# Performance work log

Measured on AMD Instinct MI355X. Metric: run time of the kernel, lower is better.

## Reference

```python
import jax, jax.numpy as jnp
import numpy as np

B, S, D = 4, 2048, 1024
H = 16
DH = D // H  # attention_head_size = 64


def setup_inputs() -> dict:
    key = jax.random.key(0)
    ks = jax.random.split(key, 7)
    scale = 0.02
    return {
        "hidden_states": jax.random.normal(ks[0], (B, S, D), dtype=jnp.float32),
        "Wq": jax.random.normal(ks[1], (D, D), dtype=jnp.float32) * scale,
        "bq": jnp.zeros((D,), dtype=jnp.float32),
        "Wk": jax.random.normal(ks[2], (D, D), dtype=jnp.float32) * scale,
        "bk": jnp.zeros((D,), dtype=jnp.float32),
        "Wv": jax.random.normal(ks[3], (D, D), dtype=jnp.float32) * scale,
        "bv": jnp.zeros((D,), dtype=jnp.float32),
    }


def _split_heads(x):
    # [B, S, D] -> [B, H, S, DH]
    b, s, _ = x.shape
    return x.reshape(b, s, H, DH).transpose(0, 2, 1, 3)


def reference(hidden_states, Wq, bq, Wk, bk, Wv, bv):
    # torch nn.Linear computes x @ W.T + b
    q = _split_heads(hidden_states @ Wq.T + bq)  # [B,H,S,DH]
    k = _split_heads(hidden_states @ Wk.T + bk)
    v = _split_heads(hidden_states @ Wv.T + bv)

    scores = jnp.einsum("bhqd,bhkd->bhqk", q, k) / jnp.sqrt(jnp.float32(DH))
    # original detaches attention probs (LRP-style)
    probs = jax.lax.stop_gradient(jax.nn.softmax(scores, axis=-1))
    ctx = jnp.einsum("bhqk,bhkd->bhqd", probs, v)  # [B,H,S,DH]
    # [B,H,S,DH] -> [B,S,D]
    return ctx.transpose(0, 2, 1, 3).reshape(hidden_states.shape[0], hidden_states.shape[1], D)
```

## Files before the change

### kernel.cpp

```cpp
#include <hip/hip_runtime.h>

typedef _Float16 f16;
typedef f16 f16x2 __attribute__((ext_vector_type(2)));
typedef f16 f16x4 __attribute__((ext_vector_type(4)));
typedef f16 f16x8 __attribute__((ext_vector_type(8)));
typedef float f32x4 __attribute__((ext_vector_type(4)));

#define NB 4
#define NS 2048
#define ND 1024
#define NH 16
#define NDH 64

__device__ __forceinline__ void gl2lds16(const void* g, void* l) {
  __builtin_amdgcn_global_load_lds(
      (const __attribute__((address_space(1))) unsigned int*)g,
      (__attribute__((address_space(3))) unsigned int*)l, 16, 0, 0);
}

__device__ __forceinline__ float fast_exp2(float x) {
  return __builtin_amdgcn_exp2f(x);
}

__device__ __forceinline__ f16x2 pk_f16(float a, float b) {
  return __builtin_bit_cast(f16x2, __builtin_amdgcn_cvt_pkrtz(a, b));
}

__global__ __launch_bounds__(256) void cvt_all(
    const float* __restrict__ X, const float* __restrict__ Wq,
    const float* __restrict__ Wk, const float* __restrict__ Wv,
    f16* __restrict__ Xh, f16* __restrict__ Wh) {
  int b = blockIdx.x;
  const float* src;
  f16* dst;
  int off;
  if (b < 8192)       { src = X;  dst = Xh;               off = 0; }
  else if (b < 9216)  { src = Wq; dst = Wh;               off = 8192; }
  else if (b < 10240) { src = Wk; dst = Wh + (1u << 20);  off = 9216; }
  else                { src = Wv; dst = Wh + (2u << 20);  off = 10240; }
  int i = (b - off) * 256 + threadIdx.x;
  float4 v = ((const float4*)src)[i];
  f16x4 h = {(f16)v.x, (f16)v.y, (f16)v.z, (f16)v.w};
  ((f16x4*)dst)[i] = h;
}

__global__ __launch_bounds__(256) void qkv_gemm(
    const f16* __restrict__ Xh, const f16* __restrict__ Wh,
    const float* __restrict__ bq, const float* __restrict__ bk,
    const float* __restrict__ bv,
    f16* __restrict__ QF, f16* __restrict__ KF, f16* __restrict__ VF) {
  __shared__ f16 Ah[128 * 64];
  __shared__ f16 Bh[128 * 64];
  const int t = threadIdx.x;
  const int tileM = blockIdx.x * 128;
  const int nGlob = blockIdx.y * 128;
  const int mat = nGlob >> 10;
  const int col0 = nGlob & 1023;
  const int wave = t >> 6, lane = t & 63;
  const int mOff = (wave & 1) * 64, nOff = (wave >> 1) * 64;
  const int lr = lane & 15, quad = lane >> 4;

  f32x4 acc[4][4];
#pragma unroll
  for (int i = 0; i < 4; i++)
#pragma unroll
    for (int j = 0; j < 4; j++) acc[i][j] = f32x4{0.f, 0.f, 0.f, 0.f};

  const int srow = t >> 3;
  const int sx = ((t & 7) ^ (srow & 7)) * 8;
  const f16* ag = Xh + (size_t)(tileM + srow) * ND + sx;
  const f16* bg = Wh + (size_t)mat * ND * ND + (size_t)(col0 + srow) * ND + sx;
  const bool qk = (mat < 2);
  const int rx = lr & 7;

  for (int kk = 0; kk < ND; kk += 64) {
    __syncthreads();
    gl2lds16(ag + kk,                       Ah + t * 8);
    gl2lds16(ag + (size_t)32 * ND + kk,     Ah + 2048 + t * 8);
    gl2lds16(ag + (size_t)64 * ND + kk,     Ah + 4096 + t * 8);
    gl2lds16(ag + (size_t)96 * ND + kk,     Ah + 6144 + t * 8);
    gl2lds16(bg + kk,                       Bh + t * 8);
    gl2lds16(bg + (size_t)32 * ND + kk,     Bh + 2048 + t * 8);
    gl2lds16(bg + (size_t)64 * ND + kk,     Bh + 4096 + t * 8);
    gl2lds16(bg + (size_t)96 * ND + kk,     Bh + 6144 + t * 8);
    __syncthreads();
#pragma unroll
    for (int c = 0; c < 2; c++) {
      const int ch = ((c * 4 + quad) ^ rx) * 8;
      f16x8 af[4], bf[4];
#pragma unroll
      for (int i = 0; i < 4; i++)
        af[i] = *(const f16x8*)(Ah + (mOff + i * 16 + lr) * 64 + ch);
#pragma unroll
      for (int j = 0; j < 4; j++)
        bf[j] = *(const f16x8*)(Bh + (nOff + j * 16 + lr) * 64 + ch);
      if (qk) {
#pragma unroll
        for (int i = 0; i < 4; i++)
#pragma unroll
          for (int j = 0; j < 4; j++)
            acc[i][j] = __builtin_amdgcn_mfma_f32_16x16x32_f16(bf[j], af[i], acc[i][j], 0, 0, 0);
      } else {
#pragma unroll
        for (int i = 0; i < 4; i++)
#pragma unroll
          for (int j = 0; j < 4; j++)
            acc[i][j] = __builtin_amdgcn_mfma_f32_16x16x32_f16(af[i], bf[j], acc[i][j], 0, 0, 0);
      }
    }
  }

  if (qk) {
    const float* bias = (mat == 0) ? bq : bk;
    f16* dst = (mat == 0) ? QF : KF;
    const float sc = (mat == 0) ? 0.18033688f : 1.0f;
    const int jstart = (quad & 1) * 4;
#pragma unroll
    for (int j = 0; j < 4; j++) {
      int n0 = col0 + nOff + j * 16;
      int h = n0 >> 6;
      int f = j >> 1;
      int lam = lr + 16 * ((2 * j + (quad >> 1)) & 3);
      float4 bb = *(const float4*)(bias + n0 + quad * 4);
#pragma unroll
      for (int i = 0; i < 4; i++) {
        int sF = tileM + mOff + i * 16;
        int b = sF >> 11, st = (sF & 2047) >> 4;
        int bh = b * NH + h;
        f16x4 v;
#pragma unroll
        for (int r = 0; r < 4; r++) v[r] = (f16)((acc[i][j][r] + (&bb.x)[r]) * sc);
        *(f16x4*)(dst + (((size_t)(bh * 128 + st) * 2 + f) * 64 + lam) * 8 + jstart) = v;
      }
    }
  } else {
#pragma unroll
    for (int j = 0; j < 4; j++) {
      int n = col0 + nOff + j * 16 + lr;
      int h = n >> 6, dt = (n >> 4) & 3;
      float bb = bv[n];
#pragma unroll
      for (int i = 0; i < 4; i++) {
        int sF = tileM + mOff + i * 16;
        int b = sF >> 11;
        int kt2 = (sF & 2047) >> 5;
        int ts = (sF >> 4) & 1;
        int bh = b * NH + h;
        f16x4 v;
#pragma unroll
        for (int r = 0; r < 4; r++) v[r] = (f16)(acc[i][j][r] + bb);
        *(f16x4*)(VF + ((size_t)(bh * 64 + kt2) * 4 + dt) * 512 +
                  (size_t)(quad * 16 + lr) * 8 + 4 * ts) = v;
      }
    }
  }
}

__global__ __launch_bounds__(256, 2) void attn_kernel(
    const f16* __restrict__ QF, const f16* __restrict__ KF,
    const f16* __restrict__ VF, float* __restrict__ out) {
  __shared__ f16 LK[3][2048];
  __shared__ f16 LV[3][2048];
  const int t = threadIdx.x, wave = t >> 6, lane = t & 63;
  const int lr = lane & 15, quad = lane >> 4;
  const int bh = blockIdx.x, qb = blockIdx.y;
  const int bb = bh >> 4, hh = bh & 15;
  const size_t bhOff = (size_t)bh * 131072;
  const f16* Qp = QF + bhOff + (size_t)lane * 8;
  const f16* Kg = KF + bhOff + (size_t)t * 8;
  const f16* Vg = VF + bhOff + (size_t)t * 8;
  const int st0 = qb * 16 + wave * 4;

  f16x8 qf[4][2];
#pragma unroll
  for (int qt = 0; qt < 4; qt++) {
    qf[qt][0] = *(const f16x8*)(Qp + (size_t)(st0 + qt) * 1024);
    qf[qt][1] = *(const f16x8*)(Qp + (size_t)(st0 + qt) * 1024 + 512);
  }

  f32x4 o[4][4];
#pragma unroll
  for (int qt = 0; qt < 4; qt++)
#pragma unroll
    for (int dt = 0; dt < 4; dt++) o[qt][dt] = f32x4{0.f, 0.f, 0.f, 0.f};
  f32x4 lacc[4];
#pragma unroll
  for (int qt = 0; qt < 4; qt++) lacc[qt] = f32x4{0.f, 0.f, 0.f, 0.f};
  const f16x8 ones8 = {(f16)1.f, (f16)1.f, (f16)1.f, (f16)1.f,
                       (f16)1.f, (f16)1.f, (f16)1.f, (f16)1.f};

  f16x8 pfP[4], vvP[4];

  gl2lds16(Kg,        &LK[0][t * 8]);
  gl2lds16(Vg,        &LV[0][t * 8]);
  gl2lds16(Kg + 2048, &LK[1][t * 8]);
  gl2lds16(Vg + 2048, &LV[1][t * 8]);
  asm volatile("s_waitcnt vmcnt(2)" ::: "memory");
  __builtin_amdgcn_s_barrier();

  {
    f16x8 kk[4];
#pragma unroll
    for (int i = 0; i < 4; i++)
      kk[i] = *(const f16x8*)(&LK[0][i * 512 + lane * 8]);
#pragma unroll
    for (int i = 0; i < 4; i++)
      vvP[i] = *(const f16x8*)(&LV[0][i * 512 + lane * 8]);
    gl2lds16(Kg + 2 * 2048, &LK[2][t * 8]);
    gl2lds16(Vg + 2 * 2048, &LV[2][t * 8]);
    f32x4 sA[4], sB[4];
#pragma unroll
    for (int qt = 0; qt < 4; qt++) {
      sA[qt] = f32x4{0.f, 0.f, 0.f, 0.f};
      sA[qt] = __builtin_amdgcn_mfma_f32_16x16x32_f16(kk[0], qf[qt][0], sA[qt], 0, 0, 0);
      sA[qt] = __builtin_amdgcn_mfma_f32_16x16x32_f16(kk[1], qf[qt][1], sA[qt], 0, 0, 0);
      sB[qt] = f32x4{0.f, 0.f, 0.f, 0.f};
      sB[qt] = __builtin_amdgcn_mfma_f32_16x16x32_f16(kk[2], qf[qt][0], sB[qt], 0, 0, 0);
      sB[qt] = __builtin_amdgcn_mfma_f32_16x16x32_f16(kk[3], qf[qt][1], sB[qt], 0, 0, 0);
    }
#pragma unroll
    for (int qt = 0; qt < 4; qt++) {
      f16x2 a0 = pk_f16(fast_exp2(sA[qt][0]), fast_exp2(sA[qt][1]));
      f16x2 a1 = pk_f16(fast_exp2(sA[qt][2]), fast_exp2(sA[qt][3]));
      f16x2 b0 = pk_f16(fast_exp2(sB[qt][0]), fast_exp2(sB[qt][1]));
      f16x2 b1 = pk_f16(fast_exp2(sB[qt][2]), fast_exp2(sB[qt][3]));
      f16x4 lo = __builtin_shufflevector(a0, a1, 0, 1, 2, 3);
      f16x4 hi = __builtin_shufflevector(b0, b1, 0, 1, 2, 3);
      pfP[qt] = __builtin_shufflevector(lo, hi, 0, 1, 2, 3, 4, 5, 6, 7);
    }
  }
  asm volatile("s_waitcnt vmcnt(2)" ::: "memory");
  __builtin_amdgcn_s_barrier();

  int cur = 1;
  for (int g = 1; g < 64; ++g) {
    f16x8 kk[4], vv[4];
#pragma unroll
    for (int i = 0; i < 4; i++)
      kk[i] = *(const f16x8*)(&LK[cur][i * 512 + lane * 8]);
#pragma unroll
    for (int i = 0; i < 4; i++)
      vv[i] = *(const f16x8*)(&LV[cur][i * 512 + lane * 8]);
    {
      int s2 = cur + 2; if (s2 >= 3) s2 -= 3;
      const size_t nk = (size_t)((g + 2) & 63) * 2048;
      gl2lds16(Kg + nk, &LK[s2][t * 8]);
      gl2lds16(Vg + nk, &LV[s2][t * 8]);
    }
    __builtin_amdgcn_s_setprio(1);
#pragma unroll
    for (int dt = 0; dt < 4; dt++)
#pragma unroll
      for (int qt = 0; qt < 4; qt++)
        o[qt][dt] = __builtin_amdgcn_mfma_f32_16x16x32_f16(pfP[qt], vvP[dt], o[qt][dt], 0, 0, 0);
#pragma unroll
    for (int qt = 0; qt < 4; qt++)
      lacc[qt] = __builtin_amdgcn_mfma_f32_16x16x32_f16(pfP[qt], ones8, lacc[qt], 0, 0, 0);
    f32x4 sA[4], sB[4];
#pragma unroll
    for (int qt = 0; qt < 4; qt++) {
      sA[qt] = f32x4{0.f, 0.f, 0.f, 0.f};
      sA[qt] = __builtin_amdgcn_mfma_f32_16x16x32_f16(kk[0], qf[qt][0], sA[qt], 0, 0, 0);
      sA[qt] = __builtin_amdgcn_mfma_f32_16x16x32_f16(kk[1], qf[qt][1], sA[qt], 0, 0, 0);
      sB[qt] = f32x4{0.f, 0.f, 0.f, 0.f};
      sB[qt] = __builtin_amdgcn_mfma_f32_16x16x32_f16(kk[2], qf[qt][0], sB[qt], 0, 0, 0);
      sB[qt] = __builtin_amdgcn_mfma_f32_16x16x32_f16(kk[3], qf[qt][1], sB[qt], 0, 0, 0);
    }
    __builtin_amdgcn_s_setprio(0);
#pragma unroll
    for (int qt = 0; qt < 4; qt++) {
      f16x2 a0 = pk_f16(fast_exp2(sA[qt][0]), fast_exp2(sA[qt][1]));
      f16x2 a1 = pk_f16(fast_exp2(sA[qt][2]), fast_exp2(sA[qt][3]));
      f16x2 b0 = pk_f16(fast_exp2(sB[qt][0]), fast_exp2(sB[qt][1]));
      f16x2 b1 = pk_f16(fast_exp2(sB[qt][2]), fast_exp2(sB[qt][3]));
      f16x4 lo = __builtin_shufflevector(a0, a1, 0, 1, 2, 3);
      f16x4 hi = __builtin_shufflevector(b0, b1, 0, 1, 2, 3);
      pfP[qt] = __builtin_shufflevector(lo, hi, 0, 1, 2, 3, 4, 5, 6, 7);
    }
#pragma unroll
    for (int i = 0; i < 4; i++) vvP[i] = vv[i];
    asm volatile("s_waitcnt vmcnt(2)" ::: "memory");
    __builtin_amdgcn_s_barrier();
    cur = (cur == 2) ? 0 : cur + 1;
  }

#pragma unroll
  for (int dt = 0; dt < 4; dt++)
#pragma unroll
    for (int qt = 0; qt < 4; qt++)
      o[qt][dt] = __builtin_amdgcn_mfma_f32_16x16x32_f16(pfP[qt], vvP[dt], o[qt][dt], 0, 0, 0);
#pragma unroll
  for (int qt = 0; qt < 4; qt++)
    lacc[qt] = __builtin_amdgcn_mfma_f32_16x16x32_f16(pfP[qt], ones8, lacc[qt], 0, 0, 0);

#pragma unroll
  for (int qt = 0; qt < 4; qt++) {
#pragma unroll
    for (int r = 0; r < 4; r++) {
      float inv = 1.0f / lacc[qt][r];
      int q = qb * 256 + wave * 64 + qt * 16 + quad * 4 + r;
#pragma unroll
      for (int dt = 0; dt < 4; dt++)
        out[((size_t)bb * NS + q) * ND + hh * 64 + dt * 16 + lr] = o[qt][dt][r] * inv;
    }
  }
}

extern "C" void kernel_launch(void* const* d_in, const int* in_sizes, int n_in,
                              void* d_out, int out_size, void* d_ws, size_t ws_size,
                              hipStream_t stream) {
  const float* X  = (const float*)d_in[0];
  const float* Wq = (const float*)d_in[1];
  const float* bq = (const float*)d_in[2];
  const float* Wk = (const float*)d_in[3];
  const float* bk = (const float*)d_in[4];
  const float* Wv = (const float*)d_in[5];
  const float* bv = (const float*)d_in[6];
  float* out = (float*)d_out;

  f16* Xh = (f16*)d_ws;
  f16* Wh = (f16*)((char*)d_ws + (size_t)(16u << 20));
  f16* QF = (f16*)((char*)d_ws + (size_t)(22u << 20));
  f16* KF = (f16*)((char*)d_ws + (size_t)(38u << 20));
  f16* VF = (f16*)((char*)d_ws + (size_t)(54u << 20));

  cvt_all<<<11264, 256, 0, stream>>>(X, Wq, Wk, Wv, Xh, Wh);
  qkv_gemm<<<dim3(64, 24), 256, 0, stream>>>(Xh, Wh, bq, bk, bv, QF, KF, VF);
  attn_kernel<<<dim3(64, 8), 256, 0, stream>>>(QF, KF, VF, out);
}
```

Measured before the change: 214.0 us.

## Triple-buffer QKV GEMM LDS tiles with async prefetch two stages ahead

Reworks the QKV projection GEMM main loop from a synchronous single-buffer K=64 step to a three-stage ring of K=32 LDS buffers. Global-to-LDS loads for step g+2 are issued before computing step g, and partial vmcnt waits plus a single barrier per iteration replace the double syncthreads. The aim is to overlap memory latency with MFMA work. It also adds a launch-bounds occupancy hint of 3 blocks per CU. The cost is more barriers per unit of K, a changed LDS swizzle, and wrap-around prefetches that load redundant data in the final iterations.

```diff
diff --git a/kernel.cpp b/kernel.cpp
--- a/kernel.cpp
+++ b/kernel.cpp
@@ -44,13 +44,13 @@
   ((f16x4*)dst)[i] = h;
 }
 
-__global__ __launch_bounds__(256) void qkv_gemm(
+__global__ __launch_bounds__(256, 3) void qkv_gemm(
     const f16* __restrict__ Xh, const f16* __restrict__ Wh,
     const float* __restrict__ bq, const float* __restrict__ bk,
     const float* __restrict__ bv,
     f16* __restrict__ QF, f16* __restrict__ KF, f16* __restrict__ VF) {
-  __shared__ f16 Ah[128 * 64];
-  __shared__ f16 Bh[128 * 64];
+  __shared__ f16 Ah[3][128 * 32];
+  __shared__ f16 Bh[3][128 * 32];
   const int t = threadIdx.x;
   const int tileM = blockIdx.x * 128;
   const int nGlob = blockIdx.y * 128;
@@ -66,48 +66,57 @@
 #pragma unroll
     for (int j = 0; j < 4; j++) acc[i][j] = f32x4{0.f, 0.f, 0.f, 0.f};
 
-  const int srow = t >> 3;
-  const int sx = ((t & 7) ^ (srow & 7)) * 8;
+  const int srow = t >> 2;
+  const int sx = ((t & 3) ^ ((srow >> 1) & 3)) * 8;
   const f16* ag = Xh + (size_t)(tileM + srow) * ND + sx;
   const f16* bg = Wh + (size_t)mat * ND * ND + (size_t)(col0 + srow) * ND + sx;
   const bool qk = (mat < 2);
-  const int rx = lr & 7;
-
-  for (int kk = 0; kk < ND; kk += 64) {
-    __syncthreads();
-    gl2lds16(ag + kk,                       Ah + t * 8);
-    gl2lds16(ag + (size_t)32 * ND + kk,     Ah + 2048 + t * 8);
-    gl2lds16(ag + (size_t)64 * ND + kk,     Ah + 4096 + t * 8);
-    gl2lds16(ag + (size_t)96 * ND + kk,     Ah + 6144 + t * 8);
-    gl2lds16(bg + kk,                       Bh + t * 8);
-    gl2lds16(bg + (size_t)32 * ND + kk,     Bh + 2048 + t * 8);
-    gl2lds16(bg + (size_t)64 * ND + kk,     Bh + 4096 + t * 8);
-    gl2lds16(bg + (size_t)96 * ND + kk,     Bh + 6144 + t * 8);
-    __syncthreads();
-#pragma unroll
-    for (int c = 0; c < 2; c++) {
-      const int ch = ((c * 4 + quad) ^ rx) * 8;
-      f16x8 af[4], bf[4];
+  const int pc = (quad ^ ((lr >> 1) & 3)) * 8;
+
+  gl2lds16(ag,                          Ah[0] + t * 8);
+  gl2lds16(ag + (size_t)64 * ND,        Ah[0] + 2048 + t * 8);
+  gl2lds16(bg,                          Bh[0] + t * 8);
+  gl2lds16(bg + (size_t)64 * ND,        Bh[0] + 2048 + t * 8);
+  gl2lds16(ag + 32,                     Ah[1] + t * 8);
+  gl2lds16(ag + (size_t)64 * ND + 32,   Ah[1] + 2048 + t * 8);
+  gl2lds16(bg + 32,                     Bh[1] + t * 8);
+  gl2lds16(bg + (size_t)64 * ND + 32,   Bh[1] + 2048 + t * 8);
+  asm volatile("s_waitcnt vmcnt(4)" ::: "memory");
+  __builtin_amdgcn_s_barrier();
+
+  int cur = 0;
+  for (int g = 0; g < 32; ++g) {
+    {
+      int s2 = cur + 2; if (s2 >= 3) s2 -= 3;
+      const size_t ko = (size_t)(((g + 2) & 31) * 32);
+      gl2lds16(ag + ko,                        Ah[s2] + t * 8);
+      gl2lds16(ag + (size_t)64 * ND + ko,      Ah[s2] + 2048 + t * 8);
+      gl2lds16(bg + ko,                        Bh[s2] + t * 8);
+      gl2lds16(bg + (size_t)64 * ND + ko,      Bh[s2] + 2048 + t * 8);
+    }
+    f16x8 af[4], bf[4];
+#pragma unroll
+    for (int i = 0; i < 4; i++)
+      af[i] = *(const f16x8*)(Ah[cur] + (mOff + i * 16 + lr) * 32 + pc);
+#pragma unroll
+    for (int j = 0; j < 4; j++)
+      bf[j] = *(const f16x8*)(Bh[cur] + (nOff + j * 16 + lr) * 32 + pc);
+    if (qk) {
 #pragma unroll
       for (int i = 0; i < 4; i++)
-        af[i] = *(const f16x8*)(Ah + (mOff + i * 16 + lr) * 64 + ch);
-#pragma unroll
-      for (int j = 0; j < 4; j++)
-        bf[j] = *(const f16x8*)(Bh + (nOff + j * 16 + lr) * 64 + ch);
-      if (qk) {
-#pragma unroll
-        for (int i = 0; i < 4; i++)
-#pragma unroll
-          for (int j = 0; j < 4; j++)
-            acc[i][j] = __builtin_amdgcn_mfma_f32_16x16x32_f16(bf[j], af[i], acc[i][j], 0, 0, 0);
-      } else {
-#pragma unroll
-        for (int i = 0; i < 4; i++)
-#pragma unroll
-          for (int j = 0; j < 4; j++)
-            acc[i][j] = __builtin_amdgcn_mfma_f32_16x16x32_f16(af[i], bf[j], acc[i][j], 0, 0, 0);
-      }
-    }
+#pragma unroll
+        for (int j = 0; j < 4; j++)
+          acc[i][j] = __builtin_amdgcn_mfma_f32_16x16x32_f16(bf[j], af[i], acc[i][j], 0, 0, 0);
+    } else {
+#pragma unroll
+      for (int i = 0; i < 4; i++)
+#pragma unroll
+        for (int j = 0; j < 4; j++)
+          acc[i][j] = __builtin_amdgcn_mfma_f32_16x16x32_f16(af[i], bf[j], acc[i][j], 0, 0, 0);
+    }
+    asm volatile("s_waitcnt vmcnt(4)" ::: "memory");
+    __builtin_amdgcn_s_barrier();
+    cur = (cur == 2) ? 0 : cur + 1;
   }
 
   if (qk) {
```

New measurement: 287.8 us. 34.5% more time.

## Double-buffer QKV GEMM LDS tiles and merge V stores into 16-byte writes

Applied to the files above, without the earlier changes.

The QKV projection GEMM now keeps two LDS buffers for the A and B tiles. It prefetches the next K-slice with global_load_lds while MFMAs run on the current one, and drops one of the two barriers per iteration. The V epilogue also packs two adjacent 16-row accumulator tiles into a single f16x8 store instead of two f16x4 stores. The cost is double the LDS use per block (64KB), which may lower occupancy. The wait on vmcnt(0) at the end of each iteration still serializes each prefetch before the next compute step.

```diff
diff --git a/kernel.cpp b/kernel.cpp
--- a/kernel.cpp
+++ b/kernel.cpp
@@ -49,8 +49,8 @@
     const float* __restrict__ bq, const float* __restrict__ bk,
     const float* __restrict__ bv,
     f16* __restrict__ QF, f16* __restrict__ KF, f16* __restrict__ VF) {
-  __shared__ f16 Ah[128 * 64];
-  __shared__ f16 Bh[128 * 64];
+  __shared__ f16 Ah[2][128 * 64];
+  __shared__ f16 Bh[2][128 * 64];
   const int t = threadIdx.x;
   const int tileM = blockIdx.x * 128;
   const int nGlob = blockIdx.y * 128;
@@ -73,27 +73,40 @@
   const bool qk = (mat < 2);
   const int rx = lr & 7;
 
-  for (int kk = 0; kk < ND; kk += 64) {
-    __syncthreads();
-    gl2lds16(ag + kk,                       Ah + t * 8);
-    gl2lds16(ag + (size_t)32 * ND + kk,     Ah + 2048 + t * 8);
-    gl2lds16(ag + (size_t)64 * ND + kk,     Ah + 4096 + t * 8);
-    gl2lds16(ag + (size_t)96 * ND + kk,     Ah + 6144 + t * 8);
-    gl2lds16(bg + kk,                       Bh + t * 8);
-    gl2lds16(bg + (size_t)32 * ND + kk,     Bh + 2048 + t * 8);
-    gl2lds16(bg + (size_t)64 * ND + kk,     Bh + 4096 + t * 8);
-    gl2lds16(bg + (size_t)96 * ND + kk,     Bh + 6144 + t * 8);
-    __syncthreads();
+  gl2lds16(ag,                       Ah[0] + t * 8);
+  gl2lds16(ag + (size_t)32 * ND,     Ah[0] + 2048 + t * 8);
+  gl2lds16(ag + (size_t)64 * ND,     Ah[0] + 4096 + t * 8);
+  gl2lds16(ag + (size_t)96 * ND,     Ah[0] + 6144 + t * 8);
+  gl2lds16(bg,                       Bh[0] + t * 8);
+  gl2lds16(bg + (size_t)32 * ND,     Bh[0] + 2048 + t * 8);
+  gl2lds16(bg + (size_t)64 * ND,     Bh[0] + 4096 + t * 8);
+  gl2lds16(bg + (size_t)96 * ND,     Bh[0] + 6144 + t * 8);
+  asm volatile("s_waitcnt vmcnt(0)" ::: "memory");
+  __builtin_amdgcn_s_barrier();
+
+  for (int kk = 0; kk < 16; ++kk) {
+    const int buf = kk & 1;
+    if (kk < 15) {
+      const size_t ko = (size_t)(kk + 1) * 64;
+      gl2lds16(ag + ko,                       Ah[buf ^ 1] + t * 8);
+      gl2lds16(ag + (size_t)32 * ND + ko,     Ah[buf ^ 1] + 2048 + t * 8);
+      gl2lds16(ag + (size_t)64 * ND + ko,     Ah[buf ^ 1] + 4096 + t * 8);
+      gl2lds16(ag + (size_t)96 * ND + ko,     Ah[buf ^ 1] + 6144 + t * 8);
+      gl2lds16(bg + ko,                       Bh[buf ^ 1] + t * 8);
+      gl2lds16(bg + (size_t)32 * ND + ko,     Bh[buf ^ 1] + 2048 + t * 8);
+      gl2lds16(bg + (size_t)64 * ND + ko,     Bh[buf ^ 1] + 4096 + t * 8);
+      gl2lds16(bg + (size_t)96 * ND + ko,     Bh[buf ^ 1] + 6144 + t * 8);
+    }
 #pragma unroll
     for (int c = 0; c < 2; c++) {
       const int ch = ((c * 4 + quad) ^ rx) * 8;
       f16x8 af[4], bf[4];
 #pragma unroll
       for (int i = 0; i < 4; i++)
-        af[i] = *(const f16x8*)(Ah + (mOff + i * 16 + lr) * 64 + ch);
+        af[i] = *(const f16x8*)(Ah[buf] + (mOff + i * 16 + lr) * 64 + ch);
 #pragma unroll
       for (int j = 0; j < 4; j++)
-        bf[j] = *(const f16x8*)(Bh + (nOff + j * 16 + lr) * 64 + ch);
+        bf[j] = *(const f16x8*)(Bh[buf] + (nOff + j * 16 + lr) * 64 + ch);
       if (qk) {
 #pragma unroll
         for (int i = 0; i < 4; i++)
@@ -108,6 +121,8 @@
             acc[i][j] = __builtin_amdgcn_mfma_f32_16x16x32_f16(af[i], bf[j], acc[i][j], 0, 0, 0);
       }
     }
+    asm volatile("s_waitcnt vmcnt(0)" ::: "memory");
+    __builtin_amdgcn_s_barrier();
   }
 
   if (qk) {
@@ -140,17 +155,20 @@
       int h = n >> 6, dt = (n >> 4) & 3;
       float bb = bv[n];
 #pragma unroll
-      for (int i = 0; i < 4; i++) {
-        int sF = tileM + mOff + i * 16;
+      for (int p = 0; p < 2; p++) {
+        int i0 = 2 * p;
+        int sF = tileM + mOff + i0 * 16;
         int b = sF >> 11;
         int kt2 = (sF & 2047) >> 5;
-        int ts = (sF >> 4) & 1;
         int bh = b * NH + h;
-        f16x4 v;
-#pragma unroll
-        for (int r = 0; r < 4; r++) v[r] = (f16)(acc[i][j][r] + bb);
-        *(f16x4*)(VF + ((size_t)(bh * 64 + kt2) * 4 + dt) * 512 +
-                  (size_t)(quad * 16 + lr) * 8 + 4 * ts) = v;
+        f16x8 v;
+#pragma unroll
+        for (int r = 0; r < 4; r++) {
+          v[r] = (f16)(acc[i0][j][r] + bb);
+          v[4 + r] = (f16)(acc[i0 + 1][j][r] + bb);
+        }
+        *(f16x8*)(VF + ((size_t)(bh * 64 + kt2) * 4 + dt) * 512 +
+                  (size_t)(quad * 16 + lr) * 8) = v;
       }
     }
   }
```

After: 215.2 us. No clear change (+0.6%).
